# Performance work log

Hardware: AMD Instinct MI355X
Metric: run time of the kernel (lower is better)

The kernel has to match this reference:

```python
import jax, jax.numpy as jnp
import numpy as np

B, C, H, W, HEADS = 16, 256, 64, 64, 4
BN_EPS = 1e-5


def setup_inputs() -> dict:
    key = jax.random.key(0)
    ks = jax.random.split(key, 6)
    sc = lambda k, shape, s: (jax.random.normal(k, shape, jnp.float32) * s)
    return {
        "x": sc(ks[0], (B, C, H, W), 1.0),
        "qkv_w": sc(ks[1], (C, C), C ** -0.5),
        "temp": jnp.ones((HEADS, 1), jnp.float32),
        "proj_w": sc(ks[2], (C, C), C ** -0.5),
        "proj_b": jnp.zeros((C,), jnp.float32),
        "conv1_w": sc(ks[3], (2 * C, C), C ** -0.5),
        "bn1_g": jnp.ones((2 * C,), jnp.float32),
        "bn1_b": jnp.zeros((2 * C,), jnp.float32),
        "bn1_m": jnp.zeros((2 * C,), jnp.float32),
        "bn1_v": jnp.ones((2 * C,), jnp.float32),
        "conv2_w": sc(ks[4], (C, 2 * C), (2 * C) ** -0.5),
        "bn2_g": jnp.ones((C,), jnp.float32),
        "bn2_b": jnp.zeros((C,), jnp.float32),
        "bn2_m": jnp.zeros((C,), jnp.float32),
        "bn2_v": jnp.ones((C,), jnp.float32),
    }


def _attention_tssa(x3, qkv_w, temp, proj_w, proj_b):
    # x3: [b, n, c]
    b, n, c = x3.shape
    d = c // HEADS
    w = (x3 @ qkv_w.T).reshape(b, n, HEADS, d).transpose(0, 2, 1, 3)  # b h n d
    # F.normalize over token dim (dim=-2), eps=1e-12
    nrm = jnp.sqrt(jnp.sum(w * w, axis=2, keepdims=True))
    w_normed = w / jnp.maximum(nrm, 1e-12)
    # logits [b, h, n]; temp is (h, 1) -> broadcast per head
    s = jnp.sum(w_normed * w_normed, axis=-1) * temp[:, 0][None, :, None]
    Pi = jax.nn.softmax(s, axis=1)  # softmax over HEAD dim (torch Softmax(dim=1))
    Pi_n = Pi / (jnp.sum(Pi, axis=-1, keepdims=True) + 1e-8)
    dots = jnp.einsum('bhn,bhnd->bhd', Pi_n, w * w)  # [b, h, d]
    attn = 1.0 / (1.0 + dots)
    out = -(w * Pi[..., None]) * attn[:, :, None, :]  # b h n d
    out = out.transpose(0, 2, 1, 3).reshape(b, n, c)
    return out @ proj_w.T + proj_b


def _bn(y, g, b_, m, v):
    scale = (g / jnp.sqrt(v + BN_EPS))[None, :, None, None]
    return (y - m[None, :, None, None]) * scale + b_[None, :, None, None]


def reference(x, qkv_w, temp, proj_w, proj_b, conv1_w, bn1_g, bn1_b, bn1_m, bn1_v,
              conv2_w, bn2_g, bn2_b, bn2_m, bn2_v):
    b, c, h, w_ = x.shape
    x3 = x.reshape(b, c, h * w_).transpose(0, 2, 1)  # b n c
    a = _attention_tssa(x3, qkv_w, temp, proj_w, proj_b)  # b n c
    x = x + a.transpose(0, 2, 1).reshape(b, c, h, w_)
    # FFN: 1x1 conv -> BN -> SiLU -> 1x1 conv -> BN (no act), residual
    y = jnp.einsum('bchw,oc->bohw', x, conv1_w)
    y = _bn(y, bn1_g, bn1_b, bn1_m, bn1_v)
    y = y * jax.nn.sigmoid(y)  # SiLU
    z = jnp.einsum('bchw,oc->bohw', y, conv2_w)
    z = _bn(z, bn2_g, bn2_b, bn2_m, bn2_v)
    return x + z
```

## Files before the change

### kernel.cpp

```cpp
#include <hip/hip_runtime.h>
#include <hip/hip_bf16.h>
#include <stdint.h>

typedef unsigned short u16;
using bf16x8 = __attribute__((ext_vector_type(8))) short;
using f32x4  = __attribute__((ext_vector_type(4))) float;

#define DEVI static __device__ __forceinline__

constexpr int CB = 16;
constexpr int CC = 256;
constexpr int CN = 4096;
constexpr int CH = 4;

DEVI u16 f2b(float f){
  union { float f; uint32_t u; } v; v.f = f;
  return (u16)((v.u + 0x7FFFu + ((v.u >> 16) & 1u)) >> 16);
}
DEVI float b2f(u16 u){
  union { uint32_t u; float f; } v; v.u = ((uint32_t)u) << 16; return v.f;
}

__global__ __launch_bounds__(256) void k_prep_w(const float* __restrict__ qkv, const float* __restrict__ pj,
    const float* __restrict__ c1, const float* __restrict__ c2,
    u16* __restrict__ qkvb, u16* __restrict__ pjb, u16* __restrict__ c1b, u16* __restrict__ c2b){
  int id = blockIdx.x * 256 + threadIdx.x;
  if (id < 65536) qkvb[id] = f2b(qkv[id]);
  else if (id < 131072) pjb[id - 65536] = f2b(pj[id - 65536]);
  else if (id < 262144) c1b[id - 131072] = f2b(c1[id - 131072]);
  else c2b[id - 262144] = f2b(c2[id - 262144]);
}

__global__ __launch_bounds__(256) void k_prep_bn(const float* __restrict__ g1,const float* __restrict__ b1,
    const float* __restrict__ m1,const float* __restrict__ v1,
    const float* __restrict__ g2,const float* __restrict__ b2,
    const float* __restrict__ m2,const float* __restrict__ v2,
    float* __restrict__ s1,float* __restrict__ o1,float* __restrict__ s2,float* __restrict__ o2){
  int id = blockIdx.x*256 + threadIdx.x;
  if (id < 512){ float s = g1[id] * rsqrtf(v1[id] + 1e-5f); s1[id] = s; o1[id] = b1[id] - m1[id]*s; }
  else if (id < 768){ int c = id - 512; float s = g2[c] * rsqrtf(v2[c] + 1e-5f); s2[c] = s; o2[c] = b2[c] - m2[c]*s; }
}

__global__ __launch_bounds__(256) void k_tr(const float* __restrict__ x, u16* __restrict__ xb){
  __shared__ float t[32][33];
  int b = blockIdx.x, c0 = blockIdx.y*32, n0 = blockIdx.z*32;
  int tr = threadIdx.x >> 5, tc = threadIdx.x & 31;
  const float* xp = x + ((size_t)b*CC + c0)*CN + n0;
  #pragma unroll
  for (int p=0;p<4;p++) t[tr + p*8][tc] = xp[(size_t)(tr + p*8)*CN + tc];
  __syncthreads();
  u16* op = xb + ((size_t)b*CN + n0)*CC + c0;
  #pragma unroll
  for (int p=0;p<4;p++) op[(size_t)(tr + p*8)*CC + tc] = f2b(t[tc][tr + p*8]);
}

template<int M_, int K_, int EPI>
__global__ __launch_bounds__(256) void k_gemm(
    const u16* __restrict__ Aw, const u16* __restrict__ Act,
    float* of, u16* __restrict__ ob,
    const float* __restrict__ e0, const float* __restrict__ e1,
    const u16* __restrict__ eb)
{
  __shared__ __align__(16) u16 As[2][128*64];
  __shared__ __align__(16) u16 Bs[2][128*64];
  const int t = threadIdx.x;
  const int lane = t & 63, wave = t >> 6;
  const int wr = wave >> 1, wc = wave & 1;
  const int lg = lane >> 4, lr = lane & 15;
  const int gx = gridDim.x, gy = gridDim.y;
  const int nwg = gx * gy * gridDim.z;
  const int id0 = blockIdx.x + gx*(blockIdx.y + gy*blockIdx.z);
  const int id  = (id0 & 7)*(nwg >> 3) + (id0 >> 3);
  const int bx = id % gx; const int rem = id / gx;
  const int by = rem % gy; const int bz = rem / gy;
  const int n0 = bx * 128, m0 = by * 128, b = bz;
  const u16* Ag = Aw + (size_t)m0 * K_;
  const u16* Bg = Act + ((size_t)b * CN + n0) * K_;
  f32x4 acc[4][4] = {};
  constexpr int NT = K_/64;
  auto stage = [&](int p, int kt){
    #pragma unroll
    for (int i=0;i<4;i++){
      int off = (i*256 + t) * 8;
      int m = off >> 6, gq = (off >> 3) & 7;
      int kk = (gq ^ (m & 7)) * 8;
      __builtin_amdgcn_global_load_lds(
        (__attribute__((address_space(1))) void*)(Ag + (size_t)m*K_ + kt*64 + kk),
        (__attribute__((address_space(3))) void*)(&As[p][(i*256 + wave*64)*8]), 16, 0, 0);
      __builtin_amdgcn_global_load_lds(
        (__attribute__((address_space(1))) void*)(Bg + (size_t)m*K_ + kt*64 + kk),
        (__attribute__((address_space(3))) void*)(&Bs[p][(i*256 + wave*64)*8]), 16, 0, 0);
    }
  };
  stage(0, 0);
  __syncthreads();
  for (int kt = 0; kt < NT; ++kt){
    const int cur = kt & 1;
    if (kt + 1 < NT) stage(cur ^ 1, kt + 1);
    #pragma unroll
    for (int s=0;s<2;s++){
      bf16x8 af[4], bfv[4];
      #pragma unroll
      for (int mi=0;mi<4;mi++){
        int r = wr*64 + mi*16 + lr;
        af[mi] = *(const bf16x8*)(&As[cur][r*64 + (((s*4+lg) ^ (r & 7)) * 8)]);
      }
      #pragma unroll
      for (int ni=0;ni<4;ni++){
        int r = wc*64 + ni*16 + lr;
        bfv[ni] = *(const bf16x8*)(&Bs[cur][r*64 + (((s*4+lg) ^ (r & 7)) * 8)]);
      }
      #pragma unroll
      for (int mi=0;mi<4;mi++)
        #pragma unroll
        for (int ni=0;ni<4;ni++)
          acc[mi][ni] = __builtin_amdgcn_mfma_f32_16x16x32_bf16(af[mi], bfv[ni], acc[mi][ni], 0, 0, 0);
    }
    __syncthreads();
  }
  #pragma unroll
  for (int mi=0;mi<4;mi++){
    const int mb = m0 + wr*64 + mi*16 + lg*4;
    float sq[4] = {0.f,0.f,0.f,0.f};
    #pragma unroll
    for (int ni=0;ni<4;ni++){
      const int n = n0 + wc*64 + ni*16 + lr;
      f32x4 v = acc[mi][ni];
      if constexpr (EPI == 0){
        ushort4 u;
        #pragma unroll
        for (int j=0;j<4;j++){ ((u16*)&u)[j] = f2b(v[j]); sq[j] += v[j]*v[j]; }
        *(ushort4*)(ob + ((size_t)b*CN + n)*M_ + mb) = u;
      } else if constexpr (EPI == 1){
        ushort4 u;
        #pragma unroll
        for (int j=0;j<4;j++){
          size_t ix = ((size_t)b*CC + mb + j)*CN + n;
          ((u16*)&u)[j] = f2b(v[j] + e0[mb + j] + e1[ix]);
        }
        *(ushort4*)(ob + ((size_t)b*CN + n)*M_ + mb) = u;
      } else if constexpr (EPI == 2){
        ushort4 u;
        #pragma unroll
        for (int j=0;j<4;j++){
          float r = v[j]*e0[mb+j] + e1[mb+j];
          r = r / (1.f + __expf(-r));
          ((u16*)&u)[j] = f2b(r);
        }
        *(ushort4*)(ob + ((size_t)b*CN + n)*M_ + mb) = u;
      } else {
        ushort4 xw = *(const ushort4*)(eb + ((size_t)b*CN + n)*M_ + mb);
        #pragma unroll
        for (int j=0;j<4;j++){
          size_t ix = ((size_t)b*CC + mb + j)*CN + n;
          of[ix] = v[j]*e0[mb+j] + e1[mb+j] + b2f(((const u16*)&xw)[j]);
        }
      }
    }
    if constexpr (EPI == 0){
      #pragma unroll
      for (int off=1; off<16; off<<=1)
        #pragma unroll
        for (int j=0;j<4;j++) sq[j] += __shfl_xor(sq[j], off);
      if (lr == 0){
        #pragma unroll
        for (int j=0;j<4;j++) atomicAdd(&of[b*CC + mb + j], sq[j]);
      }
    }
  }
}

__global__ __launch_bounds__(256) void k_stats(const u16* __restrict__ W, const float* __restrict__ nrm2,
    const float* __restrict__ temp, float* __restrict__ Pi, float* __restrict__ sumPi,
    float* __restrict__ dotsU){
  __shared__ float red[4][256];
  const int b = blockIdx.x, n0 = blockIdx.y * 64;
  const int t = threadIdx.x, lane = t & 63, wave = t >> 6;
  const int grp = lane >> 4, gl = lane & 15;
  const float th = temp[grp];
  const float4 nr = *(const float4*)(nrm2 + b*CC + 4*lane);
  const float i0 = 1.f/fmaxf(nr.x,1e-24f), i1 = 1.f/fmaxf(nr.y,1e-24f);
  const float i2 = 1.f/fmaxf(nr.z,1e-24f), i3 = 1.f/fmaxf(nr.w,1e-24f);
  float accp = 0.f, d0=0.f, d1=0.f, d2=0.f, d3=0.f;
  for (int i=0;i<16;i++){
    int n = n0 + wave*16 + i;
    ushort4 wu = *(const ushort4*)(W + ((size_t)b*CN + n)*CC + 4*lane);
    float w0=b2f(wu.x), w1=b2f(wu.y), w2=b2f(wu.z), w3=b2f(wu.w);
    float q0=w0*w0, q1=w1*w1, q2=w2*w2, q3=w3*w3;
    float s = q0*i0 + q1*i1 + q2*i2 + q3*i3;
    #pragma unroll
    for (int off=1; off<16; off<<=1) s += __shfl_xor(s, off);
    s *= th;
    float sA=__shfl(s,0), sB=__shfl(s,16), sC=__shfl(s,32), sD=__shfl(s,48);
    float mx = fmaxf(fmaxf(sA,sB), fmaxf(sC,sD));
    float eA=__expf(sA-mx), eB=__expf(sB-mx), eC=__expf(sC-mx), eD=__expf(sD-mx);
    float den = eA+eB+eC+eD;
    float pih = ((grp==0)?eA:(grp==1)?eB:(grp==2)?eC:eD)/den;
    if (gl == 0){ Pi[((size_t)b*CH + grp)*CN + n] = pih; accp += pih; }
    d0 += pih*q0; d1 += pih*q1; d2 += pih*q2; d3 += pih*q3;
  }
  if (gl == 0) atomicAdd(&sumPi[b*CH + grp], accp);
  red[wave][4*lane+0]=d0; red[wave][4*lane+1]=d1; red[wave][4*lane+2]=d2; red[wave][4*lane+3]=d3;
  __syncthreads();
  float sm = red[0][t]+red[1][t]+red[2][t]+red[3][t];
  atomicAdd(&dotsU[b*CC + t], sm);
}

__global__ __launch_bounds__(256) void k_outc(const u16* __restrict__ W, const float* __restrict__ Pi,
    const float* __restrict__ dotsU, const float* __restrict__ sumPi, u16* __restrict__ oc){
  size_t id = (size_t)blockIdx.x * 256 + threadIdx.x;
  int c = ((int)(id & 63)) * 4;
  int n = (int)((id >> 6) & (CN - 1));
  int b = (int)(id >> 18);
  int h = c >> 6;
  ushort4 wu = *(const ushort4*)(W + ((size_t)b*CN + n)*CC + c);
  float pi = Pi[((size_t)b*CH + h)*CN + n];
  float sp = sumPi[b*CH + h] + 1e-8f;
  float4 du = *(const float4*)(dotsU + b*CC + c);
  float a0 = sp/(sp + du.x), a1 = sp/(sp + du.y), a2 = sp/(sp + du.z), a3 = sp/(sp + du.w);
  ushort4 u;
  u.x = f2b(-b2f(wu.x) * pi * a0);
  u.y = f2b(-b2f(wu.y) * pi * a1);
  u.z = f2b(-b2f(wu.z) * pi * a2);
  u.w = f2b(-b2f(wu.w) * pi * a3);
  *(ushort4*)(oc + ((size_t)b*CN + n)*CC + c) = u;
}

extern "C" void kernel_launch(void* const* d_in, const int* in_sizes, int n_in,
                              void* d_out, int out_size, void* d_ws, size_t ws_size,
                              hipStream_t stream) {
  (void)in_sizes; (void)n_in; (void)out_size; (void)ws_size;
  const float* x     = (const float*)d_in[0];
  const float* qkvw  = (const float*)d_in[1];
  const float* temp  = (const float*)d_in[2];
  const float* projw = (const float*)d_in[3];
  const float* projb = (const float*)d_in[4];
  const float* c1w   = (const float*)d_in[5];
  const float* g1=(const float*)d_in[6], *b1=(const float*)d_in[7], *m1=(const float*)d_in[8], *v1=(const float*)d_in[9];
  const float* c2w   = (const float*)d_in[10];
  const float* g2=(const float*)d_in[11], *b2=(const float*)d_in[12], *m2=(const float*)d_in[13], *v2=(const float*)d_in[14];
  float* out = (float*)d_out;
  char* ws = (char*)d_ws;

  constexpr size_t MB = 1024*1024;
  u16* xb  = (u16*)(ws);
  u16* oc  = xb;
  u16* yb  = (u16*)(ws);
  u16* xrb = (u16*)(ws + 64*MB);
  u16* Wb  = (u16*)(ws + 96*MB);
  char* wts = ws + 128*MB;
  u16* qkvb = (u16*)wts;
  u16* pjb  = qkvb + 65536;
  u16* c1b  = pjb + 65536;
  u16* c2b  = c1b + 131072;
  float* s1 = (float*)(wts + 786432);
  float* o1 = s1 + 512;
  float* s2 = o1 + 512;
  float* o2 = s2 + 256;
  float* Pi = (float*)(wts + 786432 + 8192);
  float* nrm2  = Pi + (size_t)CB*CH*CN;
  float* sumPi = nrm2 + CB*CC;
  float* dotsU = sumPi + CB*CH;

  hipMemsetAsync(nrm2, 0, (size_t)(CB*CC + CB*CH + CB*CC)*4, stream);
  k_prep_w<<<1536, 256, 0, stream>>>(qkvw, projw, c1w, c2w, qkvb, pjb, c1b, c2b);
  k_prep_bn<<<3, 256, 0, stream>>>(g1,b1,m1,v1,g2,b2,m2,v2,s1,o1,s2,o2);
  k_tr<<<dim3(CB, CC/32, CN/32), 256, 0, stream>>>(x, xb);
  k_gemm<256,256,0><<<dim3(CN/128, 2, CB), 256, 0, stream>>>(qkvb, xb, nrm2, Wb, nullptr, nullptr, nullptr);
  k_stats<<<dim3(CB, CN/64), 256, 0, stream>>>(Wb, nrm2, temp, Pi, sumPi, dotsU);
  k_outc<<<(CB*CN*CC/4)/256, 256, 0, stream>>>(Wb, Pi, dotsU, sumPi, oc);
  k_gemm<256,256,1><<<dim3(CN/128, 2, CB), 256, 0, stream>>>(pjb, oc, nullptr, xrb, projb, x, nullptr);
  k_gemm<512,256,2><<<dim3(CN/128, 4, CB), 256, 0, stream>>>(c1b, xrb, nullptr, yb, s1, o1, nullptr);
  k_gemm<256,512,3><<<dim3(CN/128, 2, CB), 256, 0, stream>>>(c2b, yb, out, nullptr, s2, o2, xrb);
}
```

Before: 215.5 us.

## Restructure GEMM main loop into two-deep prefetch with register-staged fragments

The GEMM main loop now keeps two K-tiles in flight. It uses explicit vmcnt waits and raw s_barrier instead of __syncthreads. Each iteration loads both k-substeps of A/B fragments into registers, waits on lgkmcnt, then barriers and issues the next tile's global-to-LDS load into the buffer it just read. The MFMAs then run at raised wave priority. Global offsets are hoisted out of the staging lambda. The aim is to hide global load latency and separate LDS reads from MFMA issue, at the cost of more registers and hand-tuned waitcnt counts that must match the number of outstanding loads.

```diff
diff --git a/kernel.cpp b/kernel.cpp
--- a/kernel.cpp
+++ b/kernel.cpp
@@ -7,6 +7,8 @@
 using f32x4  = __attribute__((ext_vector_type(4))) float;
 
 #define DEVI static __device__ __forceinline__
+#define AS1 __attribute__((address_space(1)))
+#define AS3 __attribute__((address_space(3)))
 
 constexpr int CB = 16;
 constexpr int CC = 256;
@@ -78,45 +80,56 @@
   const u16* Bg = Act + ((size_t)b * CN + n0) * K_;
   f32x4 acc[4][4] = {};
   constexpr int NT = K_/64;
+  int goff[4], ldst[4];
+  #pragma unroll
+  for (int i=0;i<4;i++){
+    int off = (i*256 + t) * 8;
+    int m = off >> 6, gq = (off >> 3) & 7;
+    int kk = (gq ^ (m & 7)) * 8;
+    goff[i] = m*K_ + kk;
+    ldst[i] = (i*256 + wave*64)*8;
+  }
   auto stage = [&](int p, int kt){
     #pragma unroll
     for (int i=0;i<4;i++){
-      int off = (i*256 + t) * 8;
-      int m = off >> 6, gq = (off >> 3) & 7;
-      int kk = (gq ^ (m & 7)) * 8;
-      __builtin_amdgcn_global_load_lds(
-        (__attribute__((address_space(1))) void*)(Ag + (size_t)m*K_ + kt*64 + kk),
-        (__attribute__((address_space(3))) void*)(&As[p][(i*256 + wave*64)*8]), 16, 0, 0);
-      __builtin_amdgcn_global_load_lds(
-        (__attribute__((address_space(1))) void*)(Bg + (size_t)m*K_ + kt*64 + kk),
-        (__attribute__((address_space(3))) void*)(&Bs[p][(i*256 + wave*64)*8]), 16, 0, 0);
+      __builtin_amdgcn_global_load_lds((AS1 void*)(Ag + goff[i] + kt*64),
+                                       (AS3 void*)(&As[p][ldst[i]]), 16, 0, 0);
+      __builtin_amdgcn_global_load_lds((AS1 void*)(Bg + goff[i] + kt*64),
+                                       (AS3 void*)(&Bs[p][ldst[i]]), 16, 0, 0);
     }
   };
   stage(0, 0);
-  __syncthreads();
+  stage(1, 1);
   for (int kt = 0; kt < NT; ++kt){
     const int cur = kt & 1;
-    if (kt + 1 < NT) stage(cur ^ 1, kt + 1);
+    if (kt + 1 < NT) { asm volatile("s_waitcnt vmcnt(8)" ::: "memory"); }
+    else             { asm volatile("s_waitcnt vmcnt(0)" ::: "memory"); }
+    __builtin_amdgcn_s_barrier();
+    __builtin_amdgcn_sched_barrier(0);
+    bf16x8 af[2][4], bfv[2][4];
     #pragma unroll
     for (int s=0;s<2;s++){
-      bf16x8 af[4], bfv[4];
       #pragma unroll
       for (int mi=0;mi<4;mi++){
         int r = wr*64 + mi*16 + lr;
-        af[mi] = *(const bf16x8*)(&As[cur][r*64 + (((s*4+lg) ^ (r & 7)) * 8)]);
+        af[s][mi] = *(const bf16x8*)(&As[cur][r*64 + (((s*4+lg) ^ (r & 7)) * 8)]);
+        int r2 = wc*64 + mi*16 + lr;
+        bfv[s][mi] = *(const bf16x8*)(&Bs[cur][r2*64 + (((s*4+lg) ^ (r2 & 7)) * 8)]);
       }
-      #pragma unroll
-      for (int ni=0;ni<4;ni++){
-        int r = wc*64 + ni*16 + lr;
-        bfv[ni] = *(const bf16x8*)(&Bs[cur][r*64 + (((s*4+lg) ^ (r & 7)) * 8)]);
-      }
+    }
+    asm volatile("s_waitcnt lgkmcnt(0)" ::: "memory");
+    __builtin_amdgcn_sched_barrier(0);
+    __builtin_amdgcn_s_barrier();
+    if (kt + 2 < NT) stage(cur, kt + 2);
+    __builtin_amdgcn_s_setprio(1);
+    #pragma unroll
+    for (int s=0;s<2;s++)
       #pragma unroll
       for (int mi=0;mi<4;mi++)
         #pragma unroll
         for (int ni=0;ni<4;ni++)
-          acc[mi][ni] = __builtin_amdgcn_mfma_f32_16x16x32_bf16(af[mi], bfv[ni], acc[mi][ni], 0, 0, 0);
-    }
-    __syncthreads();
+          acc[mi][ni] = __builtin_amdgcn_mfma_f32_16x16x32_bf16(af[s][mi], bfv[s][ni], acc[mi][ni], 0, 0, 0);
+    __builtin_amdgcn_s_setprio(0);
   }
   #pragma unroll
   for (int mi=0;mi<4;mi++){
```

Result: no change. 216.3 us (+0.4%).
